# Performance work log

Measured on AMD Instinct MI355X. Metric: run time of the kernel, lower is better.

## Reference

```python
import jax, jax.numpy as jnp
import numpy as np

B, N1, N2, D = 8, 2048, 2048, 512

def setup_inputs() -> dict:
    key = jax.random.key(0)
    k1, k2, k3, k4 = jax.random.split(key, 4)
    input1 = jax.random.normal(k1, (B, N1, D), dtype=jnp.float32)
    input2 = jax.random.normal(k2, (B, N2, D), dtype=jnp.float32)
    # nn.Linear(D, D): weight [D, D] (out, in), bias [D]
    W_w = jax.random.normal(k3, (D, D), dtype=jnp.float32) * (1.0 / np.sqrt(D))
    W_b = jax.random.normal(k4, (D,), dtype=jnp.float32) * 0.01
    return {"input1": input1, "input2": input2, "W_w": W_w, "W_b": W_b}

def reference(input1, input2, W_w, W_b):
    # q = W(input1): [B, N1, D]
    q = jnp.einsum('bnd,od->bno', input1, W_w) + W_b
    # unscaled scores softmax over last dim (keys N2)
    attn = jax.nn.softmax(jnp.einsum('bnd,bmd->bnm', q, input2), axis=-1)  # [B, N1, N2]
    output1 = jnp.einsum('bnm,bmd->bnd', attn, input2)   # [B, N1, D]
    output2 = jnp.einsum('bnm,bnd->bmd', attn, input1)   # attn^T @ input1 -> [B, N2, D]
    return (output1, output2)
```

## Files before the change

kernel.cpp:

```cpp
#include <hip/hip_runtime.h>


typedef _Float16 f16x8 __attribute__((ext_vector_type(8)));
typedef float floatx4 __attribute__((ext_vector_type(4)));
typedef __attribute__((address_space(1))) const void* gptr_t;
typedef __attribute__((address_space(3))) void* lptr_t;

union F8 { f16x8 v; _Float16 h[8]; unsigned short u[8]; unsigned w[4]; };

__device__ __forceinline__ void gld16(const void* g, void* l) {
    __builtin_amdgcn_global_load_lds((gptr_t)g, (lptr_t)l, 16, 0, 0);
}
__device__ __forceinline__ floatx4 mfma16(f16x8 a, f16x8 b, floatx4 c) {
    return __builtin_amdgcn_mfma_f32_16x16x32_f16(a, b, c, 0, 0, 0);
}

template <int ROWS>
__device__ __forceinline__ void stage64(const _Float16* g, int ldg,
                                        _Float16* lds, int tid) {
#pragma unroll
    for (int c = 0; c < (ROWS * 8) / 256; ++c) {
        const int q = c * 256 + tid;
        const int row = q >> 3;
        const int oct = (q & 7) ^ (row & 7);
        gld16(g + (size_t)row * ldg + oct * 8, lds + q * 8);
    }
}
__device__ __forceinline__ f16x8 ldfrag(const _Float16* lds, int row, int j) {
    return *(const f16x8*)&lds[row * 64 + ((j ^ (row & 7)) << 3)];
}

__global__ __launch_bounds__(256) void k_prep(const float* __restrict__ src,
                                              _Float16* __restrict__ rowo,
                                              _Float16* __restrict__ colo)
{
    const int b = blockIdx.z;
    const int d0 = blockIdx.x * 128, n0 = blockIdx.y * 32;
    const float* Sp = src + (size_t)b * 2048 * 512;
    _Float16* Rp = rowo + (size_t)b * 2048 * 512;
    _Float16* Cp = colo + (size_t)b * 512 * 2048;
    const int t = threadIdx.x, i = t & 63, jn = t >> 6;
    const int d = d0 + 2 * i, n = n0 + jn * 8;
    F8 w0, w1;
#pragma unroll
    for (int j = 0; j < 8; j++) {
        float2 g = *(const float2*)(Sp + (size_t)(n + j) * 512 + d);
        w0.h[j] = (_Float16)g.x; w1.h[j] = (_Float16)g.y;
        F8 r; r.h[0] = w0.h[j]; r.h[1] = w1.h[j];
        *(unsigned*)(Rp + (size_t)(n + j) * 512 + d) = r.w[0];
    }
    *(f16x8*)(Cp + (size_t)d * 2048 + n) = w0.v;
    *(f16x8*)(Cp + (size_t)(d + 1) * 2048 + n) = w1.v;
}

__global__ __launch_bounds__(256) void k_cvt(const float* __restrict__ src,
                                             _Float16* __restrict__ dst)
{
    const size_t i = ((size_t)blockIdx.x * 256 + threadIdx.x) * 8;
    float4 a = *(const float4*)(src + i);
    float4 b = *(const float4*)(src + i + 4);
    F8 w;
    w.h[0] = (_Float16)a.x; w.h[1] = (_Float16)a.y;
    w.h[2] = (_Float16)a.z; w.h[3] = (_Float16)a.w;
    w.h[4] = (_Float16)b.x; w.h[5] = (_Float16)b.y;
    w.h[6] = (_Float16)b.z; w.h[7] = (_Float16)b.w;
    *(f16x8*)(dst + i) = w.v;
}

__global__ __launch_bounds__(256, 4) void k_qgemm16(
    const _Float16* __restrict__ A, const _Float16* __restrict__ W,
    const float* __restrict__ bias, _Float16* __restrict__ q)
{
    __shared__ __align__(16) _Float16 As[128 * 64], Bs[128 * 64];
    const int tid = threadIdx.x;
    const int lane = tid & 63, wave = tid >> 6;
    const int wM = (wave >> 1) * 64, wN = (wave & 1) * 64;
    const int lrow = lane & 15, kq = lane >> 4;
    const int bi = blockIdx.x;
    const int r0 = (bi >> 2) * 128, c0 = (bi & 3) * 128;

    floatx4 acc[4][4];
#pragma unroll
    for (int i = 0; i < 4; i++)
#pragma unroll
        for (int j = 0; j < 4; j++) acc[i][j] = (floatx4){0.f, 0.f, 0.f, 0.f};

    for (int k0 = 0; k0 < 512; k0 += 64) {
        stage64<128>(A + (size_t)r0 * 512 + k0, 512, As, tid);
        stage64<128>(W + (size_t)c0 * 512 + k0, 512, Bs, tid);
        __syncthreads();
#pragma unroll
        for (int ks = 0; ks < 2; ks++) {
            f16x8 a[4], b[4];
#pragma unroll
            for (int i = 0; i < 4; i++) {
                a[i] = ldfrag(As, wM + i * 16 + lrow, ks * 4 + kq);
                b[i] = ldfrag(Bs, wN + i * 16 + lrow, ks * 4 + kq);
            }
#pragma unroll
            for (int mi = 0; mi < 4; mi++)
#pragma unroll
                for (int ni = 0; ni < 4; ni++)
                    acc[mi][ni] = mfma16(a[mi], b[ni], acc[mi][ni]);
        }
        __syncthreads();
    }
#pragma unroll
    for (int ni = 0; ni < 4; ni++) {
        const int col = c0 + wN + ni * 16 + lrow;
        const float bv = bias[col];
#pragma unroll
        for (int mi = 0; mi < 4; mi++) {
            const int row = r0 + wM + mi * 16 + kq * 4;
#pragma unroll
            for (int r = 0; r < 4; r++)
                q[(size_t)(row + r) * 512 + col] = (_Float16)(acc[mi][ni][r] + bv);
        }
    }
}

__global__ __launch_bounds__(256, 4) void k_scores16(
    const _Float16* __restrict__ q, const _Float16* __restrict__ k,
    _Float16* __restrict__ S)
{
    __shared__ __align__(16) _Float16 As[128 * 64], Bs[128 * 64];
    const int tid = threadIdx.x;
    const int lane = tid & 63, wave = tid >> 6;
    const int wM = (wave >> 1) * 64, wN = (wave & 1) * 64;
    const int lrow = lane & 15, kq = lane >> 4;
    const int bi = blockIdx.x;
    const int bz = bi & 3, t = bi >> 2;
    const int c0 = (t & 15) * 128, r0 = (t >> 4) * 128;
    const _Float16* qp = q + (size_t)bz * 2048 * 512;
    const _Float16* kp = k + (size_t)bz * 2048 * 512;
    _Float16* Sp = S + (size_t)bz * 2048 * 2048;

    floatx4 acc[4][4];
#pragma unroll
    for (int i = 0; i < 4; i++)
#pragma unroll
        for (int j = 0; j < 4; j++) acc[i][j] = (floatx4){0.f, 0.f, 0.f, 0.f};

    for (int k0 = 0; k0 < 512; k0 += 64) {
        stage64<128>(qp + (size_t)r0 * 512 + k0, 512, As, tid);
        stage64<128>(kp + (size_t)c0 * 512 + k0, 512, Bs, tid);
        __syncthreads();
#pragma unroll
        for (int ks = 0; ks < 2; ks++) {
            f16x8 a[4], b[4];
#pragma unroll
            for (int i = 0; i < 4; i++) {
                a[i] = ldfrag(As, wM + i * 16 + lrow, ks * 4 + kq);
                b[i] = ldfrag(Bs, wN + i * 16 + lrow, ks * 4 + kq);
            }
#pragma unroll
            for (int mi = 0; mi < 4; mi++)
#pragma unroll
                for (int ni = 0; ni < 4; ni++)
                    acc[mi][ni] = mfma16(a[mi], b[ni], acc[mi][ni]);
        }
        __syncthreads();
    }
#pragma unroll
    for (int mi = 0; mi < 4; mi++)
#pragma unroll
        for (int ni = 0; ni < 4; ni++) {
            const int row = r0 + wM + mi * 16 + kq * 4;
            const int col = c0 + wN + ni * 16 + lrow;
            _Float16* dst = Sp + (size_t)row * 2048 + col;
#pragma unroll
            for (int r = 0; r < 4; r++) dst[(size_t)r * 2048] = (_Float16)acc[mi][ni][r];
        }
}

__global__ __launch_bounds__(256) void k_softmax(const _Float16* __restrict__ S,
                                                 _Float16* __restrict__ P)
{
    const int row = blockIdx.x;
    const _Float16* s = S + (size_t)row * 2048;
    _Float16* p = P + (size_t)row * 2048;
    const int tid = threadIdx.x;
    const int lane = tid & 63, wave = tid >> 6;

    F8 raw;
    raw.v = *(const f16x8*)(s + tid * 8);
    float v[8];
#pragma unroll
    for (int i = 0; i < 8; i++) v[i] = (float)raw.h[i];
    float m = fmaxf(fmaxf(fmaxf(v[0], v[1]), fmaxf(v[2], v[3])),
                    fmaxf(fmaxf(v[4], v[5]), fmaxf(v[6], v[7])));
#pragma unroll
    for (int off = 32; off >= 1; off >>= 1) m = fmaxf(m, __shfl_down(m, off));
    __shared__ float rb[4];
    if (lane == 0) rb[wave] = m;
    __syncthreads();
    m = fmaxf(fmaxf(rb[0], rb[1]), fmaxf(rb[2], rb[3]));

    float e[8];
#pragma unroll
    for (int i = 0; i < 8; i++) e[i] = __expf(v[i] - m);
    float sum = ((e[0] + e[1]) + (e[2] + e[3])) + ((e[4] + e[5]) + (e[6] + e[7]));
#pragma unroll
    for (int off = 32; off >= 1; off >>= 1) sum += __shfl_down(sum, off);
    __syncthreads();
    if (lane == 0) rb[wave] = sum;
    __syncthreads();
    const float inv = 1.0f / (((rb[0] + rb[1]) + (rb[2] + rb[3])));

    F8 w;
#pragma unroll
    for (int i = 0; i < 8; i++) w.h[i] = (_Float16)(e[i] * inv);
    *(f16x8*)(p + tid * 8) = w.v;
}

__global__ __launch_bounds__(256, 4) void k_out1(
    const _Float16* __restrict__ P, const _Float16* __restrict__ Vt,
    float* __restrict__ O)
{
    __shared__ __align__(16) _Float16 As[64 * 64], Bs[128 * 64];
    const int tid = threadIdx.x;
    const int lane = tid & 63, wave = tid >> 6;
    const int wM = (wave >> 1) * 32, wN = (wave & 1) * 64;
    const int lrow = lane & 15, kq = lane >> 4;
    const int bi = blockIdx.x;
    const int bz = bi & 7, t = bi >> 3;
    const int c0 = (t & 3) * 128, r0 = (t >> 2) * 64;
    const _Float16* Pp = P + (size_t)bz * 2048 * 2048;
    const _Float16* Vp = Vt + (size_t)bz * 512 * 2048;
    float* Op = O + (size_t)bz * 2048 * 512;

    floatx4 acc[2][4];
#pragma unroll
    for (int i = 0; i < 2; i++)
#pragma unroll
        for (int j = 0; j < 4; j++) acc[i][j] = (floatx4){0.f, 0.f, 0.f, 0.f};

    for (int k0 = 0; k0 < 2048; k0 += 64) {
        stage64<64>(Pp + (size_t)r0 * 2048 + k0, 2048, As, tid);
        stage64<128>(Vp + (size_t)c0 * 2048 + k0, 2048, Bs, tid);
        __syncthreads();
#pragma unroll
        for (int ks = 0; ks < 2; ks++) {
            f16x8 a[2], b[4];
#pragma unroll
            for (int i = 0; i < 2; i++) a[i] = ldfrag(As, wM + i * 16 + lrow, ks * 4 + kq);
#pragma unroll
            for (int i = 0; i < 4; i++) b[i] = ldfrag(Bs, wN + i * 16 + lrow, ks * 4 + kq);
#pragma unroll
            for (int mi = 0; mi < 2; mi++)
#pragma unroll
                for (int ni = 0; ni < 4; ni++)
                    acc[mi][ni] = mfma16(a[mi], b[ni], acc[mi][ni]);
        }
        __syncthreads();
    }
#pragma unroll
    for (int mi = 0; mi < 2; mi++)
#pragma unroll
        for (int ni = 0; ni < 4; ni++) {
            const int row = r0 + wM + mi * 16 + kq * 4;
            const int col = c0 + wN + ni * 16 + lrow;
            float* dst = Op + (size_t)row * 512 + col;
#pragma unroll
            for (int r = 0; r < 4; r++) dst[(size_t)r * 512] = acc[mi][ni][r];
        }
}

#define ASTR 72
__global__ __launch_bounds__(256, 4) void k_out2(
    const _Float16* __restrict__ P, const _Float16* __restrict__ Xt,
    float* __restrict__ O)
{
    __shared__ __align__(16) _Float16 As[64 * ASTR];
    __shared__ __align__(16) _Float16 Bs[128 * 64];
    const int tid = threadIdx.x;
    const int lane = tid & 63, wave = tid >> 6;
    const int wM = (wave >> 1) * 32, wN = (wave & 1) * 64;
    const int lrow = lane & 15, kq = lane >> 4;
    const int bi = blockIdx.x;
    const int bz = bi & 7, t = bi >> 3;
    const int c0 = (t & 3) * 128, r0 = (t >> 2) * 64;
    const _Float16* Pp = P + (size_t)bz * 2048 * 2048;
    const _Float16* Xp = Xt + (size_t)bz * 512 * 2048;
    float* Op = O + (size_t)bz * 2048 * 512;

    const int mPair = (tid & 31) * 2;
    const int kOct = tid >> 5;
    const int aswz = (kOct ^ (tid & 7)) << 3;

    floatx4 acc[2][4];
#pragma unroll
    for (int i = 0; i < 2; i++)
#pragma unroll
        for (int j = 0; j < 4; j++) acc[i][j] = (floatx4){0.f, 0.f, 0.f, 0.f};

    for (int k0 = 0; k0 < 2048; k0 += 64) {
        stage64<128>(Xp + (size_t)c0 * 2048 + k0, 2048, Bs, tid);
        {
            F8 w0, w1;
#pragma unroll
            for (int j = 0; j < 8; j++) {
                const unsigned g = *(const unsigned*)(
                    Pp + (size_t)(k0 + kOct * 8 + j) * 2048 + r0 + mPair);
                w0.u[j] = (unsigned short)(g & 0xffffu);
                w1.u[j] = (unsigned short)(g >> 16);
            }
            *(f16x8*)&As[mPair * ASTR + aswz] = w0.v;
            *(f16x8*)&As[(mPair + 1) * ASTR + aswz] = w1.v;
        }
        __syncthreads();
#pragma unroll
        for (int ks = 0; ks < 2; ks++) {
            f16x8 a[2], b[4];
#pragma unroll
            for (int i = 0; i < 2; i++) {
                const int m = wM + i * 16 + lrow;
                a[i] = *(const f16x8*)&As[m * ASTR +
                                          (((ks * 4 + kq) ^ ((m >> 1) & 7)) << 3)];
            }
#pragma unroll
            for (int i = 0; i < 4; i++) b[i] = ldfrag(Bs, wN + i * 16 + lrow, ks * 4 + kq);
#pragma unroll
            for (int mi = 0; mi < 2; mi++)
#pragma unroll
                for (int ni = 0; ni < 4; ni++)
                    acc[mi][ni] = mfma16(a[mi], b[ni], acc[mi][ni]);
        }
        __syncthreads();
    }
#pragma unroll
    for (int mi = 0; mi < 2; mi++)
#pragma unroll
        for (int ni = 0; ni < 4; ni++) {
            const int row = r0 + wM + mi * 16 + kq * 4;
            const int col = c0 + wN + ni * 16 + lrow;
            float* dst = Op + (size_t)row * 512 + col;
#pragma unroll
            for (int r = 0; r < 4; r++) dst[(size_t)r * 512] = acc[mi][ni][r];
        }
}

extern "C" void kernel_launch(void* const* d_in, const int* in_sizes, int n_in,
                              void* d_out, int out_size, void* d_ws, size_t ws_size,
                              hipStream_t stream)
{
    (void)in_sizes; (void)n_in; (void)out_size; (void)ws_size;
    const float* in1 = (const float*)d_in[0];
    const float* in2 = (const float*)d_in[1];
    const float* Ww  = (const float*)d_in[2];
    const float* Wb  = (const float*)d_in[3];
    float* out = (float*)d_out;

    char* ws = (char*)d_ws;
    _Float16* S   = (_Float16*)ws;
    _Float16* P   = (_Float16*)(ws + 33554432ull);
    _Float16* q16 = (_Float16*)(ws + 100663296ull);
    _Float16* x16 = (_Float16*)(ws + 117440512ull);
    _Float16* k16 = (_Float16*)(ws + 134217728ull);
    _Float16* vt  = (_Float16*)(ws + 150994944ull);
    _Float16* xt  = (_Float16*)(ws + 167772160ull);
    _Float16* w16 = (_Float16*)(ws + 184549376ull);

    k_prep<<<dim3(4, 64, 8), 256, 0, stream>>>(in1, x16, xt);
    k_prep<<<dim3(4, 64, 8), 256, 0, stream>>>(in2, k16, vt);
    k_cvt <<<128, 256, 0, stream>>>(Ww, w16);
    k_qgemm16<<<512, 256, 0, stream>>>(x16, w16, Wb, q16);
    for (int h = 0; h < 2; h++) {
        k_scores16<<<1024, 256, 0, stream>>>(
            q16 + (size_t)h * 4 * 2048 * 512, k16 + (size_t)h * 4 * 2048 * 512, S);
        k_softmax<<<8192, 256, 0, stream>>>(S, P + (size_t)h * 4 * 2048 * 2048);
    }
    k_out1<<<1024, 256, 0, stream>>>(P, vt, out);
    k_out2<<<1024, 256, 0, stream>>>(P, xt, out + 8388608);
}
```

Baseline: 314.9 us.

## Merge launches and deepen K tile to 128 in output GEMMs

Merges the two prep conversions into one launch, runs scores and softmax over all 8 batches in single launches (growing the S workspace), and fuses the out1/out2 GEMMs into one 2048-block kernel. The output GEMMs now stage 128-wide K tiles with a 16-way XOR swizzle, halving the number of barrier iterations. The aim is to cut launch count and tail effects and let the two output GEMMs overlap. In exchange, LDS per block grows and the occupancy hint drops to 3 blocks, and the out2 path loses its XOR swizzle in favour of padding alone.

```diff
diff --git a/kernel.cpp b/kernel.cpp
--- a/kernel.cpp
+++ b/kernel.cpp
@@ -26,15 +26,35 @@
         gld16(g + (size_t)row * ldg + oct * 8, lds + q * 8);
     }
 }
-__device__ __forceinline__ f16x8 ldfrag(const _Float16* lds, int row, int j) {
+__device__ __forceinline__ f16x8 ldfrag64(const _Float16* lds, int row, int j) {
     return *(const f16x8*)&lds[row * 64 + ((j ^ (row & 7)) << 3)];
 }
 
-__global__ __launch_bounds__(256) void k_prep(const float* __restrict__ src,
-                                              _Float16* __restrict__ rowo,
-                                              _Float16* __restrict__ colo)
-{
-    const int b = blockIdx.z;
+template <int ROWS>
+__device__ __forceinline__ void stage128(const _Float16* g, int ldg,
+                                         _Float16* lds, int tid) {
+#pragma unroll
+    for (int c = 0; c < (ROWS * 16) / 256; ++c) {
+        const int q = c * 256 + tid;
+        const int row = q >> 4;
+        const int oct = (q & 15) ^ (row & 15);
+        gld16(g + (size_t)row * ldg + oct * 8, lds + q * 8);
+    }
+}
+__device__ __forceinline__ f16x8 ldfrag128(const _Float16* lds, int row, int j) {
+    return *(const f16x8*)&lds[row * 128 + ((j ^ (row & 15)) << 3)];
+}
+
+__global__ __launch_bounds__(256) void k_prep2(
+    const float* __restrict__ in1, const float* __restrict__ in2,
+    _Float16* __restrict__ x16, _Float16* __restrict__ xt,
+    _Float16* __restrict__ k16, _Float16* __restrict__ vt)
+{
+    const int z = blockIdx.z;
+    const int b = z & 7;
+    const float* src = (z < 8 ? in1 : in2);
+    _Float16* rowo = (z < 8 ? x16 : k16);
+    _Float16* colo = (z < 8 ? xt : vt);
     const int d0 = blockIdx.x * 128, n0 = blockIdx.y * 32;
     const float* Sp = src + (size_t)b * 2048 * 512;
     _Float16* Rp = rowo + (size_t)b * 2048 * 512;
@@ -94,8 +114,8 @@
             f16x8 a[4], b[4];
 #pragma unroll
             for (int i = 0; i < 4; i++) {
-                a[i] = ldfrag(As, wM + i * 16 + lrow, ks * 4 + kq);
-                b[i] = ldfrag(Bs, wN + i * 16 + lrow, ks * 4 + kq);
+                a[i] = ldfrag64(As, wM + i * 16 + lrow, ks * 4 + kq);
+                b[i] = ldfrag64(Bs, wN + i * 16 + lrow, ks * 4 + kq);
             }
 #pragma unroll
             for (int mi = 0; mi < 4; mi++)
@@ -129,7 +149,7 @@
     const int wM = (wave >> 1) * 64, wN = (wave & 1) * 64;
     const int lrow = lane & 15, kq = lane >> 4;
     const int bi = blockIdx.x;
-    const int bz = bi & 3, t = bi >> 2;
+    const int bz = bi & 7, t = bi >> 3;
     const int c0 = (t & 15) * 128, r0 = (t >> 4) * 128;
     const _Float16* qp = q + (size_t)bz * 2048 * 512;
     const _Float16* kp = k + (size_t)bz * 2048 * 512;
@@ -150,8 +170,8 @@
             f16x8 a[4], b[4];
 #pragma unroll
             for (int i = 0; i < 4; i++) {
-                a[i] = ldfrag(As, wM + i * 16 + lrow, ks * 4 + kq);
-                b[i] = ldfrag(Bs, wN + i * 16 + lrow, ks * 4 + kq);
+                a[i] = ldfrag64(As, wM + i * 16 + lrow, ks * 4 + kq);
+                b[i] = ldfrag64(Bs, wN + i * 16 + lrow, ks * 4 + kq);
             }
 #pragma unroll
             for (int mi = 0; mi < 4; mi++)
@@ -213,21 +233,25 @@
     *(f16x8*)(p + tid * 8) = w.v;
 }
 
-__global__ __launch_bounds__(256, 4) void k_out1(
+#define ASTR 136
+__global__ __launch_bounds__(256, 3) void k_out12(
     const _Float16* __restrict__ P, const _Float16* __restrict__ Vt,
-    float* __restrict__ O)
-{
-    __shared__ __align__(16) _Float16 As[64 * 64], Bs[128 * 64];
+    const _Float16* __restrict__ Xt, float* __restrict__ O1,
+    float* __restrict__ O2)
+{
+    __shared__ __align__(16) _Float16 As[64 * ASTR];
+    __shared__ __align__(16) _Float16 Bs[128 * 128];
     const int tid = threadIdx.x;
     const int lane = tid & 63, wave = tid >> 6;
     const int wM = (wave >> 1) * 32, wN = (wave & 1) * 64;
     const int lrow = lane & 15, kq = lane >> 4;
-    const int bi = blockIdx.x;
+    const bool isO2 = blockIdx.x >= 1024;
+    const int bi = blockIdx.x & 1023;
     const int bz = bi & 7, t = bi >> 3;
     const int c0 = (t & 3) * 128, r0 = (t >> 2) * 64;
     const _Float16* Pp = P + (size_t)bz * 2048 * 2048;
-    const _Float16* Vp = Vt + (size_t)bz * 512 * 2048;
-    float* Op = O + (size_t)bz * 2048 * 512;
+    const _Float16* Bp = (isO2 ? Xt : Vt) + (size_t)bz * 512 * 2048;
+    float* Op = (isO2 ? O2 : O1) + (size_t)bz * 2048 * 512;
 
     floatx4 acc[2][4];
 #pragma unroll
@@ -235,98 +259,66 @@
 #pragma unroll
         for (int j = 0; j < 4; j++) acc[i][j] = (floatx4){0.f, 0.f, 0.f, 0.f};
 
-    for (int k0 = 0; k0 < 2048; k0 += 64) {
-        stage64<64>(Pp + (size_t)r0 * 2048 + k0, 2048, As, tid);
-        stage64<128>(Vp + (size_t)c0 * 2048 + k0, 2048, Bs, tid);
-        __syncthreads();
-#pragma unroll
-        for (int ks = 0; ks < 2; ks++) {
-            f16x8 a[2], b[4];
-#pragma unroll
-            for (int i = 0; i < 2; i++) a[i] = ldfrag(As, wM + i * 16 + lrow, ks * 4 + kq);
-#pragma unroll
-            for (int i = 0; i < 4; i++) b[i] = ldfrag(Bs, wN + i * 16 + lrow, ks * 4 + kq);
-#pragma unroll
-            for (int mi = 0; mi < 2; mi++)
-#pragma unroll
-                for (int ni = 0; ni < 4; ni++)
-                    acc[mi][ni] = mfma16(a[mi], b[ni], acc[mi][ni]);
-        }
-        __syncthreads();
-    }
-#pragma unroll
-    for (int mi = 0; mi < 2; mi++)
-#pragma unroll
-        for (int ni = 0; ni < 4; ni++) {
-            const int row = r0 + wM + mi * 16 + kq * 4;
-            const int col = c0 + wN + ni * 16 + lrow;
-            float* dst = Op + (size_t)row * 512 + col;
-#pragma unroll
-            for (int r = 0; r < 4; r++) dst[(size_t)r * 512] = acc[mi][ni][r];
-        }
-}
-
-#define ASTR 72
-__global__ __launch_bounds__(256, 4) void k_out2(
-    const _Float16* __restrict__ P, const _Float16* __restrict__ Xt,
-    float* __restrict__ O)
-{
-    __shared__ __align__(16) _Float16 As[64 * ASTR];
-    __shared__ __align__(16) _Float16 Bs[128 * 64];
-    const int tid = threadIdx.x;
-    const int lane = tid & 63, wave = tid >> 6;
-    const int wM = (wave >> 1) * 32, wN = (wave & 1) * 64;
-    const int lrow = lane & 15, kq = lane >> 4;
-    const int bi = blockIdx.x;
-    const int bz = bi & 7, t = bi >> 3;
-    const int c0 = (t & 3) * 128, r0 = (t >> 2) * 64;
-    const _Float16* Pp = P + (size_t)bz * 2048 * 2048;
-    const _Float16* Xp = Xt + (size_t)bz * 512 * 2048;
-    float* Op = O + (size_t)bz * 2048 * 512;
-
-    const int mPair = (tid & 31) * 2;
-    const int kOct = tid >> 5;
-    const int aswz = (kOct ^ (tid & 7)) << 3;
-
-    floatx4 acc[2][4];
-#pragma unroll
-    for (int i = 0; i < 2; i++)
-#pragma unroll
-        for (int j = 0; j < 4; j++) acc[i][j] = (floatx4){0.f, 0.f, 0.f, 0.f};
-
-    for (int k0 = 0; k0 < 2048; k0 += 64) {
-        stage64<128>(Xp + (size_t)c0 * 2048 + k0, 2048, Bs, tid);
-        {
-            F8 w0, w1;
-#pragma unroll
-            for (int j = 0; j < 8; j++) {
-                const unsigned g = *(const unsigned*)(
-                    Pp + (size_t)(k0 + kOct * 8 + j) * 2048 + r0 + mPair);
-                w0.u[j] = (unsigned short)(g & 0xffffu);
-                w1.u[j] = (unsigned short)(g >> 16);
-            }
-            *(f16x8*)&As[mPair * ASTR + aswz] = w0.v;
-            *(f16x8*)&As[(mPair + 1) * ASTR + aswz] = w1.v;
-        }
-        __syncthreads();
-#pragma unroll
-        for (int ks = 0; ks < 2; ks++) {
-            f16x8 a[2], b[4];
-#pragma unroll
-            for (int i = 0; i < 2; i++) {
-                const int m = wM + i * 16 + lrow;
-                a[i] = *(const f16x8*)&As[m * ASTR +
-                                          (((ks * 4 + kq) ^ ((m >> 1) & 7)) << 3)];
-            }
-#pragma unroll
-            for (int i = 0; i < 4; i++) b[i] = ldfrag(Bs, wN + i * 16 + lrow, ks * 4 + kq);
-#pragma unroll
-            for (int mi = 0; mi < 2; mi++)
-#pragma unroll
-                for (int ni = 0; ni < 4; ni++)
-                    acc[mi][ni] = mfma16(a[mi], b[ni], acc[mi][ni]);
-        }
-        __syncthreads();
+    if (!isO2) {
+        for (int k0 = 0; k0 < 2048; k0 += 128) {
+            stage128<64>(Pp + (size_t)r0 * 2048 + k0, 2048, As, tid);
+            stage128<128>(Bp + (size_t)c0 * 2048 + k0, 2048, Bs, tid);
+            __syncthreads();
+#pragma unroll
+            for (int ks = 0; ks < 4; ks++) {
+                f16x8 a[2], b[4];
+#pragma unroll
+                for (int i = 0; i < 2; i++)
+                    a[i] = ldfrag128(As, wM + i * 16 + lrow, ks * 4 + kq);
+#pragma unroll
+                for (int i = 0; i < 4; i++)
+                    b[i] = ldfrag128(Bs, wN + i * 16 + lrow, ks * 4 + kq);
+#pragma unroll
+                for (int mi = 0; mi < 2; mi++)
+#pragma unroll
+                    for (int ni = 0; ni < 4; ni++)
+                        acc[mi][ni] = mfma16(a[mi], b[ni], acc[mi][ni]);
+            }
+            __syncthreads();
+        }
+    } else {
+        const int mPair = (tid & 31) * 2;
+        const int kOct0 = tid >> 5;
+        for (int k0 = 0; k0 < 2048; k0 += 128) {
+            stage128<128>(Bp + (size_t)c0 * 2048 + k0, 2048, Bs, tid);
+#pragma unroll
+            for (int kh = 0; kh < 2; kh++) {
+                const int kOct = kOct0 + kh * 8;
+                F8 w0, w1;
+#pragma unroll
+                for (int j = 0; j < 8; j++) {
+                    const unsigned g = *(const unsigned*)(
+                        Pp + (size_t)(k0 + kOct * 8 + j) * 2048 + r0 + mPair);
+                    w0.u[j] = (unsigned short)(g & 0xffffu);
+                    w1.u[j] = (unsigned short)(g >> 16);
+                }
+                *(f16x8*)&As[mPair * ASTR + kOct * 8] = w0.v;
+                *(f16x8*)&As[(mPair + 1) * ASTR + kOct * 8] = w1.v;
+            }
+            __syncthreads();
+#pragma unroll
+            for (int ks = 0; ks < 4; ks++) {
+                f16x8 a[2], b[4];
+#pragma unroll
+                for (int i = 0; i < 2; i++)
+                    a[i] = *(const f16x8*)&As[(wM + i * 16 + lrow) * ASTR +
+                                              (ks * 4 + kq) * 8];
+#pragma unroll
+                for (int i = 0; i < 4; i++)
+                    b[i] = ldfrag128(Bs, wN + i * 16 + lrow, ks * 4 + kq);
+#pragma unroll
+                for (int mi = 0; mi < 2; mi++)
+#pragma unroll
+                    for (int ni = 0; ni < 4; ni++)
+                        acc[mi][ni] = mfma16(a[mi], b[ni], acc[mi][ni]);
+            }
+            __syncthreads();
+        }
     }
 #pragma unroll
     for (int mi = 0; mi < 2; mi++)
@@ -353,23 +345,18 @@
 
     char* ws = (char*)d_ws;
     _Float16* S   = (_Float16*)ws;
-    _Float16* P   = (_Float16*)(ws + 33554432ull);
-    _Float16* q16 = (_Float16*)(ws + 100663296ull);
-    _Float16* x16 = (_Float16*)(ws + 117440512ull);
-    _Float16* k16 = (_Float16*)(ws + 134217728ull);
-    _Float16* vt  = (_Float16*)(ws + 150994944ull);
-    _Float16* xt  = (_Float16*)(ws + 167772160ull);
-    _Float16* w16 = (_Float16*)(ws + 184549376ull);
-
-    k_prep<<<dim3(4, 64, 8), 256, 0, stream>>>(in1, x16, xt);
-    k_prep<<<dim3(4, 64, 8), 256, 0, stream>>>(in2, k16, vt);
+    _Float16* P   = (_Float16*)(ws + 67108864ull);
+    _Float16* q16 = (_Float16*)(ws + 134217728ull);
+    _Float16* x16 = (_Float16*)(ws + 150994944ull);
+    _Float16* k16 = (_Float16*)(ws + 167772160ull);
+    _Float16* vt  = (_Float16*)(ws + 184549376ull);
+    _Float16* xt  = (_Float16*)(ws + 201326592ull);
+    _Float16* w16 = (_Float16*)(ws + 218103808ull);
+
+    k_prep2<<<dim3(4, 64, 16), 256, 0, stream>>>(in1, in2, x16, xt, k16, vt);
     k_cvt <<<128, 256, 0, stream>>>(Ww, w16);
     k_qgemm16<<<512, 256, 0, stream>>>(x16, w16, Wb, q16);
-    for (int h = 0; h < 2; h++) {
-        k_scores16<<<1024, 256, 0, stream>>>(
-            q16 + (size_t)h * 4 * 2048 * 512, k16 + (size_t)h * 4 * 2048 * 512, S);
-        k_softmax<<<8192, 256, 0, stream>>>(S, P + (size_t)h * 4 * 2048 * 2048);
-    }
-    k_out1<<<1024, 256, 0, stream>>>(P, vt, out);
-    k_out2<<<1024, 256, 0, stream>>>(P, xt, out + 8388608);
-}
+    k_scores16<<<2048, 256, 0, stream>>>(q16, k16, S);
+    k_softmax<<<16384, 256, 0, stream>>>(S, P);
+    k_out12<<<2048, 256, 0, stream>>>(P, vt, xt, out, out + 8388608);
+}
```

Result: faster. 291.8 us (-7.3%).
